# Kernel tuning notes

Measured on AMD Instinct MI355X. Metric: run time of the kernel, lower is better.

Reference implementation:

```python
import jax, jax.numpy as jnp
import numpy as np

N_STEPS = 25
H_DIM = 64


def _gru_cell(x_in, h, Wk, Uk, b):
    # Keras GRU v2 (reset_after=True):
    # x gates: x @ Wk + b[0]; h gates: h @ Uk + b[1]
    xg = x_in @ Wk + b[0]          # (B, 3H)
    hg = h @ Uk + b[1]             # (B, 3H)
    xz, xr, xh = jnp.split(xg, 3, axis=-1)
    hz, hr, hh = jnp.split(hg, 3, axis=-1)
    z = jax.nn.sigmoid(xz + hz)
    r = jax.nn.sigmoid(xr + hr)
    cand = jnp.tanh(xh + r * hh)
    return z * h + (1.0 - z) * cand


def setup_inputs() -> dict:
    key = jax.random.key(0)
    ks = jax.random.split(key, 6)
    B = 32768
    return {
        "x": jax.random.normal(ks[0], (B, 128), jnp.float32),
        "H": jax.random.normal(ks[1], (B, 64), jnp.float32),
        "Wk": jax.random.normal(ks[2], (128, 192), jnp.float32) * 0.05,
        "Uk": jax.random.normal(ks[3], (64, 192), jnp.float32) * 0.05,
        "b": jnp.zeros((2, 192), jnp.float32),
        "Wd": jax.random.normal(ks[4], (64, 78), jnp.float32) * 0.05,
        "bd": jnp.zeros((78,), jnp.float32),
    }


def reference(x, H, Wk, Uk, b, Wd, bd):
    # Step 0: 128-dim decoder input from x[1][:,0,0,:128].
    h1 = _gru_cell(x, H, Wk, Uk, b)
    # Steps 1..24: the 64-dim GRU output is fed back as the input; this is
    # equivalent to zero-padding it to 128 dims, i.e. using Wk[:64].
    Wk64 = Wk[:H_DIM]

    def body(h, _):
        hn = _gru_cell(h, h, Wk64, Uk, b)
        return hn, hn

    _, hs = jax.lax.scan(body, h1, None, length=N_STEPS - 1)  # (24, B, 64)
    outs = jnp.concatenate([h1[None], hs], axis=0)            # (25, B, 64)
    outs = jnp.transpose(outs, (1, 0, 2))                     # (B, 25, 64)
    logits = outs @ Wd + bd                                   # (B, 25, 78)
    return jax.nn.softmax(logits, axis=-1)
```

## Files before the change

### kernel.cpp

```cpp
#include <hip/hip_runtime.h>


typedef _Float16 f16x8 __attribute__((ext_vector_type(8)));
typedef float f32x4 __attribute__((ext_vector_type(4)));

#define TPB 512
#define LOG2E 1.44269504088896f
#define S2E   2.88539008177793f

template <int CTRL>
__device__ __forceinline__ float dppror(float x) {
  return __int_as_float(
      __builtin_amdgcn_update_dpp(0, __float_as_int(x), CTRL, 0xf, 0xf, true));
}
__device__ __forceinline__ void split8h(const float f[8], f16x8& hi, f16x8& lo) {
  #pragma unroll
  for (int j = 0; j < 8; ++j) {
    _Float16 h = (_Float16)f[j];
    hi[j] = h;
    lo[j] = (_Float16)(f[j] - (float)h);
  }
}

#define MFMA __builtin_amdgcn_mfma_f32_16x16x32_f16
#define EXP2 __builtin_amdgcn_exp2f
#define RCP  __builtin_amdgcn_rcpf

__global__ __launch_bounds__(TPB, 2) void vgru_all(
    const float* __restrict__ x, const float* __restrict__ Hin,
    const float* __restrict__ Wk, const float* __restrict__ Uk,
    const float* __restrict__ bias, const float* __restrict__ Wd,
    const float* __restrict__ bd, float* __restrict__ out)
{
  extern __shared__ float smem[];
  float* chkAll = smem;
  unsigned short* hs = (unsigned short*)(smem + 24576);

  const int tid  = threadIdx.x;
  const int lane = tid & 63, w = tid >> 6;
  const int g = lane >> 4, n = lane & 15;
  const int blockbase = blockIdx.x * 128;
  const int myrow0 = blockbase + w * 16;
  const float* b0 = bias;
  const float* b1 = bias + 192;

  float bb[16];
  #pragma unroll
  for (int jt = 0; jt < 4; ++jt) {
    int c = jt * 16 + n;
    bb[0 * 4 + jt] = (b0[c] + b1[c]) * LOG2E;
    bb[1 * 4 + jt] = (b0[64 + c] + b1[64 + c]) * LOG2E;
    bb[2 * 4 + jt] = b0[128 + c] * S2E;
    bb[3 * 4 + jt] = b1[128 + c] * S2E;
  }
  float bdv[5];
  #pragma unroll
  for (int nt = 0; nt < 5; ++nt) {
    int c = nt * 16 + n;
    bdv[nt] = (c < 78) ? bd[c] * LOG2E : 0.0f;
  }

  for (int idx = tid; idx < 96 * 64; idx += TPB) {
    int fi = idx >> 6, ln = idx & 63;
    int t = fi >> 4, ntb = fi & 15;
    int lg = ln >> 4, lnn = ln & 15;
    int c = ntb * 16 + lnn;
    float scale = (c < 128) ? LOG2E : S2E;
    f16x8 wf;
    #pragma unroll
    for (int j = 0; j < 8; ++j) {
      int k = t * 32 + lg * 8 + j;
      float v;
      if (k < 128) v = (c < 192) ? Wk[k * 192 + c] : 0.0f;
      else {
        int ku = k - 128;
        v = (c < 128) ? Uk[ku * 192 + c]
                      : ((c < 192) ? 0.0f : Uk[ku * 192 + 128 + (c - 192)]);
      }
      wf[j] = (_Float16)(v * scale);
    }
    ((f16x8*)chkAll)[fi * 64 + ln] = wf;
  }
  __syncthreads();

  f32x4 G0[16];
  #pragma unroll
  for (int ntb = 0; ntb < 16; ++ntb) {
    float bv = bb[ntb];
    G0[ntb] = (f32x4){bv, bv, bv, bv};
  }
  #pragma unroll 1
  for (int t = 0; t < 6; ++t) {
    f16x8 Ah, Al;
    {
      int row = myrow0 + n;
      const float* src = (t < 4)
          ? x + (size_t)row * 128 + t * 32 + g * 8
          : Hin + (size_t)row * 64 + (t - 4) * 32 + g * 8;
      float4 v0 = *(const float4*)src;
      float4 v1 = *(const float4*)(src + 4);
      float f[8] = {v0.x, v0.y, v0.z, v0.w, v1.x, v1.y, v1.z, v1.w};
      split8h(f, Ah, Al);
    }
    __builtin_amdgcn_s_setprio(1);
    #pragma unroll
    for (int ntb = 0; ntb < 16; ++ntb) {
      f16x8 wf = ((const f16x8*)chkAll)[(t * 16 + ntb) * 64 + lane];
      G0[ntb] = MFMA(Ah, wf, G0[ntb], 0, 0, 0);
      G0[ntb] = MFMA(Al, wf, G0[ntb], 0, 0, 0);
    }
    __builtin_amdgcn_s_setprio(0);
  }

  float hold[16];
  {
    unsigned short* h0 = hs + w * 2048;
    #pragma unroll
    for (int jt = 0; jt < 4; ++jt) {
      const int ksw = jt >> 1;
      const int gkw = (jt & 1) * 2 + (n >> 3);
      const int jw  = n & 7;
      #pragma unroll
      for (int rr = 0; rr < 4; ++rr) {
        int lrow = g * 4 + rr;
        float h0v = Hin[(size_t)(myrow0 + lrow) * 64 + jt * 16 + n];
        float z  = RCP(1.0f + EXP2(-G0[0 * 4 + jt][rr]));
        float rg = RCP(1.0f + EXP2(-G0[1 * 4 + jt][rr]));
        float y  = G0[2 * 4 + jt][rr] + rg * G0[3 * 4 + jt][rr];
        float cand = 1.0f - 2.0f * RCP(EXP2(y) + 1.0f);
        float hv = cand + z * (h0v - cand);
        hold[jt * 4 + rr] = hv;
        int off = ((ksw * 4 + gkw) * 16 + lrow) * 8 + jw;
        h0[off] = __builtin_bit_cast(unsigned short, (_Float16)hv);
      }
    }
  }
  __syncthreads();

  for (int idx = tid; idx < 2048; idx += TPB) {
    int fi = idx >> 6, ln = idx & 63;
    int ntb = fi >> 1, ks = fi & 1;
    int lg = ln >> 4, lnn = ln & 15;
    int c = ntb * 16 + lnn;
    float scale = (c < 128) ? LOG2E : S2E;
    f16x8 wf;
    #pragma unroll
    for (int j = 0; j < 8; ++j) {
      int k = ks * 32 + lg * 8 + j;
      float v;
      if      (c < 128) v = Wk[k * 192 + c] + Uk[k * 192 + c];
      else if (c < 192) v = Wk[k * 192 + c];
      else              v = Uk[k * 192 + 128 + (c - 192)];
      wf[j] = (_Float16)(v * scale);
    }
    ((f16x8*)smem)[fi * 64 + ln] = wf;
  }
  for (int idx = tid; idx < 640; idx += TPB) {
    int fi = idx >> 6, ln = idx & 63;
    int nt = fi >> 1, ks = fi & 1;
    int lg = ln >> 4, lnn = ln & 15;
    int c = nt * 16 + lnn;
    f16x8 wf;
    #pragma unroll
    for (int j = 0; j < 8; ++j) {
      int k = ks * 32 + lg * 8 + j;
      wf[j] = (_Float16)((c < 78) ? Wd[k * 78 + c] * LOG2E : 0.0f);
    }
    ((f16x8*)(smem + 8192))[fi * 64 + ln] = wf;
  }
  __syncthreads();

  const f16x8* GW = (const f16x8*)smem;
  f16x8 wdr[5][2];
  #pragma unroll
  for (int nt = 0; nt < 5; ++nt)
    #pragma unroll
    for (int ks = 0; ks < 2; ++ks)
      wdr[nt][ks] = ((const f16x8*)(smem + 8192))[(nt * 2 + ks) * 64 + lane];

  float* op0 = out + ((size_t)(myrow0 + g * 4 + 0) * 25) * 78 + n;
  float* op1 = out + ((size_t)(myrow0 + g * 4 + 1) * 25) * 78 + n;
  float* op2 = out + ((size_t)(myrow0 + g * 4 + 2) * 25) * 78 + n;
  float* op3 = out + ((size_t)(myrow0 + g * 4 + 3) * 25) * 78 + n;

  f16x8 Ah[2];
  {
    const unsigned short* c0 = hs + w * 2048;
    #pragma unroll
    for (int ks = 0; ks < 2; ++ks) {
      int off = ((ks * 4 + g) * 16 + n) * 8;
      Ah[ks] = *(const f16x8*)(c0 + off);
    }
  }

  #pragma unroll 1
  for (int s = 0; s < 25; ++s) {
    unsigned short* nxt = hs + w * 2048 + ((s + 1) & 1) * 1024;
    const bool last = (s == 24);

    f32x4 C[4][4];
    #pragma unroll
    for (int jt = 0; jt < 4; ++jt)
      #pragma unroll
      for (int gg = 0; gg < 4; ++gg) {
        float bv = bb[gg * 4 + jt];
        C[jt][gg] = (f32x4){bv, bv, bv, bv};
      }
    f32x4 L[5];
    #pragma unroll
    for (int nt = 0; nt < 5; ++nt)
      L[nt] = (f32x4){bdv[nt], bdv[nt], bdv[nt], bdv[nt]};

    __builtin_amdgcn_s_setprio(1);
    if (!last) {
      #pragma unroll
      for (int jt = 0; jt < 4; ++jt)
        #pragma unroll
        for (int ks = 0; ks < 2; ++ks) {
          f16x8 w0 = GW[((0 * 4 + jt) * 2 + ks) * 64 + lane];
          f16x8 w1 = GW[((1 * 4 + jt) * 2 + ks) * 64 + lane];
          f16x8 w2 = GW[((2 * 4 + jt) * 2 + ks) * 64 + lane];
          f16x8 w3 = GW[((3 * 4 + jt) * 2 + ks) * 64 + lane];
          C[jt][0] = MFMA(Ah[ks], w0, C[jt][0], 0, 0, 0);
          C[jt][1] = MFMA(Ah[ks], w1, C[jt][1], 0, 0, 0);
          C[jt][2] = MFMA(Ah[ks], w2, C[jt][2], 0, 0, 0);
          C[jt][3] = MFMA(Ah[ks], w3, C[jt][3], 0, 0, 0);
        }
    }
    #pragma unroll
    for (int nt = 0; nt < 5; ++nt)
      #pragma unroll
      for (int ks = 0; ks < 2; ++ks)
        L[nt] = MFMA(Ah[ks], wdr[nt][ks], L[nt], 0, 0, 0);
    __builtin_amdgcn_s_setprio(0);

    if (!last) {
      #pragma unroll
      for (int jt = 0; jt < 4; ++jt) {
        const int ksw = jt >> 1;
        const int gkw = (jt & 1) * 2 + (n >> 3);
        const int jw  = n & 7;
        #pragma unroll
        for (int rr = 0; rr < 4; ++rr) {
          float z  = RCP(1.0f + EXP2(-C[jt][0][rr]));
          float rg = RCP(1.0f + EXP2(-C[jt][1][rr]));
          float y  = C[jt][2][rr] + rg * C[jt][3][rr];
          float cand = 1.0f - 2.0f * RCP(EXP2(y) + 1.0f);
          float hv = cand + z * (hold[jt * 4 + rr] - cand);
          hold[jt * 4 + rr] = hv;
          int off = ((ksw * 4 + gkw) * 16 + (g * 4 + rr)) * 8 + jw;
          nxt[off] = __builtin_bit_cast(unsigned short, (_Float16)hv);
        }
      }
      #pragma unroll
      for (int ks = 0; ks < 2; ++ks) {
        int off = ((ks * 4 + g) * 16 + n) * 8;
        Ah[ks] = *(const f16x8*)(nxt + off);
      }
    }

    #pragma unroll
    for (int rr = 0; rr < 4; ++rr) {
      float e0 = EXP2(L[0][rr]);
      float e1 = EXP2(L[1][rr]);
      float e2 = EXP2(L[2][rr]);
      float e3 = EXP2(L[3][rr]);
      float e4 = (n < 14) ? EXP2(L[4][rr]) : 0.0f;
      float sm = e0 + e1 + e2 + e3 + e4;
      sm += dppror<0x128>(sm);
      sm += dppror<0x124>(sm);
      sm += dppror<0x122>(sm);
      sm += dppror<0x121>(sm);
      float inv = RCP(sm);
      float* orow = (rr == 0) ? op0 : (rr == 1) ? op1 : (rr == 2) ? op2 : op3;
      orow[0]  = e0 * inv;
      orow[16] = e1 * inv;
      orow[32] = e2 * inv;
      orow[48] = e3 * inv;
      if (n < 14) orow[64] = e4 * inv;
    }
    op0 += 78; op1 += 78; op2 += 78; op3 += 78;
  }
}

extern "C" void kernel_launch(void* const* d_in, const int* in_sizes, int n_in,
                              void* d_out, int out_size, void* d_ws, size_t ws_size,
                              hipStream_t stream) {
  const float* x   = (const float*)d_in[0];
  const float* H   = (const float*)d_in[1];
  const float* Wk  = (const float*)d_in[2];
  const float* Uk  = (const float*)d_in[3];
  const float* b   = (const float*)d_in[4];
  const float* Wd  = (const float*)d_in[5];
  const float* bd  = (const float*)d_in[6];
  float* out = (float*)d_out;
  (void)d_ws; (void)ws_size; (void)in_sizes; (void)n_in; (void)out_size;

  const int lds = 32768 * 4;
  hipFuncSetAttribute((const void*)vgru_all,
                      hipFuncAttributeMaxDynamicSharedMemorySize, lds);
  vgru_all<<<dim3(256), dim3(TPB), lds, stream>>>(x, H, Wk, Uk, b, Wd, bd, out);
}
```

Before: 112.5 us.

## Keep GRU recurrent weights in registers and split gate MFMAs into two halves

The 32 recurrent-gate weight fragments are loaded from shared memory into registers once, before the 25-step loop, instead of being re-read from LDS every step. The dense-layer weights, previously held in registers, are now read from LDS each step. Within a step, the gate MFMAs and activations are processed in two halves, so each half's transcendental math can overlap the other half's MFMAs and fewer accumulators are live at once. The cost is much higher VGPR use from 32 f16x8 weight registers, which may lower occupancy or cause spills.

```diff
diff --git a/kernel.cpp b/kernel.cpp
--- a/kernel.cpp
+++ b/kernel.cpp
@@ -91,7 +91,7 @@
   }
   #pragma unroll 1
   for (int t = 0; t < 6; ++t) {
-    f16x8 Ah, Al;
+    f16x8 Ah0, Al0;
     {
       int row = myrow0 + n;
       const float* src = (t < 4)
@@ -100,14 +100,14 @@
       float4 v0 = *(const float4*)src;
       float4 v1 = *(const float4*)(src + 4);
       float f[8] = {v0.x, v0.y, v0.z, v0.w, v1.x, v1.y, v1.z, v1.w};
-      split8h(f, Ah, Al);
+      split8h(f, Ah0, Al0);
     }
     __builtin_amdgcn_s_setprio(1);
     #pragma unroll
     for (int ntb = 0; ntb < 16; ++ntb) {
       f16x8 wf = ((const f16x8*)chkAll)[(t * 16 + ntb) * 64 + lane];
-      G0[ntb] = MFMA(Ah, wf, G0[ntb], 0, 0, 0);
-      G0[ntb] = MFMA(Al, wf, G0[ntb], 0, 0, 0);
+      G0[ntb] = MFMA(Ah0, wf, G0[ntb], 0, 0, 0);
+      G0[ntb] = MFMA(Al0, wf, G0[ntb], 0, 0, 0);
     }
     __builtin_amdgcn_s_setprio(0);
   }
@@ -170,13 +170,16 @@
   }
   __syncthreads();
 
-  const f16x8* GW = (const f16x8*)smem;
-  f16x8 wdr[5][2];
-  #pragma unroll
-  for (int nt = 0; nt < 5; ++nt)
-    #pragma unroll
-    for (int ks = 0; ks < 2; ++ks)
-      wdr[nt][ks] = ((const f16x8*)(smem + 8192))[(nt * 2 + ks) * 64 + lane];
+  f16x8 Wg[4][4][2];
+  #pragma unroll
+  for (int gg = 0; gg < 4; ++gg)
+    #pragma unroll
+    for (int jt = 0; jt < 4; ++jt)
+      #pragma unroll
+      for (int ks = 0; ks < 2; ++ks)
+        Wg[gg][jt][ks] = ((const f16x8*)smem)[((gg * 4 + jt) * 2 + ks) * 64 + lane];
+
+  const f16x8* WD = (const f16x8*)(smem + 8192);
 
   float* op0 = out + ((size_t)(myrow0 + g * 4 + 0) * 25) * 78 + n;
   float* op1 = out + ((size_t)(myrow0 + g * 4 + 1) * 25) * 78 + n;
@@ -198,58 +201,59 @@
     unsigned short* nxt = hs + w * 2048 + ((s + 1) & 1) * 1024;
     const bool last = (s == 24);
 
-    f32x4 C[4][4];
-    #pragma unroll
-    for (int jt = 0; jt < 4; ++jt)
-      #pragma unroll
-      for (int gg = 0; gg < 4; ++gg) {
-        float bv = bb[gg * 4 + jt];
-        C[jt][gg] = (f32x4){bv, bv, bv, bv};
-      }
     f32x4 L[5];
     #pragma unroll
     for (int nt = 0; nt < 5; ++nt)
       L[nt] = (f32x4){bdv[nt], bdv[nt], bdv[nt], bdv[nt]};
-
     __builtin_amdgcn_s_setprio(1);
+    #pragma unroll
+    for (int nt = 0; nt < 5; ++nt)
+      #pragma unroll
+      for (int ks = 0; ks < 2; ++ks)
+        L[nt] = MFMA(Ah[ks], WD[(nt * 2 + ks) * 64 + lane], L[nt], 0, 0, 0);
+    __builtin_amdgcn_s_setprio(0);
+
     if (!last) {
       #pragma unroll
-      for (int jt = 0; jt < 4; ++jt)
+      for (int jp = 0; jp < 2; ++jp) {
+        f32x4 C[2][4];
         #pragma unroll
-        for (int ks = 0; ks < 2; ++ks) {
-          f16x8 w0 = GW[((0 * 4 + jt) * 2 + ks) * 64 + lane];
-          f16x8 w1 = GW[((1 * 4 + jt) * 2 + ks) * 64 + lane];
-          f16x8 w2 = GW[((2 * 4 + jt) * 2 + ks) * 64 + lane];
-          f16x8 w3 = GW[((3 * 4 + jt) * 2 + ks) * 64 + lane];
-          C[jt][0] = MFMA(Ah[ks], w0, C[jt][0], 0, 0, 0);
-          C[jt][1] = MFMA(Ah[ks], w1, C[jt][1], 0, 0, 0);
-          C[jt][2] = MFMA(Ah[ks], w2, C[jt][2], 0, 0, 0);
-          C[jt][3] = MFMA(Ah[ks], w3, C[jt][3], 0, 0, 0);
+        for (int jl = 0; jl < 2; ++jl)
+          #pragma unroll
+          for (int gg = 0; gg < 4; ++gg) {
+            float bv = bb[gg * 4 + (jp * 2 + jl)];
+            C[jl][gg] = (f32x4){bv, bv, bv, bv};
+          }
+        __builtin_amdgcn_s_setprio(1);
+        #pragma unroll
+        for (int jl = 0; jl < 2; ++jl) {
+          const int jt = jp * 2 + jl;
+          #pragma unroll
+          for (int ks = 0; ks < 2; ++ks) {
+            C[jl][0] = MFMA(Ah[ks], Wg[0][jt][ks], C[jl][0], 0, 0, 0);
+            C[jl][1] = MFMA(Ah[ks], Wg[1][jt][ks], C[jl][1], 0, 0, 0);
+            C[jl][2] = MFMA(Ah[ks], Wg[2][jt][ks], C[jl][2], 0, 0, 0);
+            C[jl][3] = MFMA(Ah[ks], Wg[3][jt][ks], C[jl][3], 0, 0, 0);
+          }
         }
-    }
-    #pragma unroll
-    for (int nt = 0; nt < 5; ++nt)
-      #pragma unroll
-      for (int ks = 0; ks < 2; ++ks)
-        L[nt] = MFMA(Ah[ks], wdr[nt][ks], L[nt], 0, 0, 0);
-    __builtin_amdgcn_s_setprio(0);
-
-    if (!last) {
-      #pragma unroll
-      for (int jt = 0; jt < 4; ++jt) {
-        const int ksw = jt >> 1;
-        const int gkw = (jt & 1) * 2 + (n >> 3);
-        const int jw  = n & 7;
+        __builtin_amdgcn_s_setprio(0);
         #pragma unroll
-        for (int rr = 0; rr < 4; ++rr) {
-          float z  = RCP(1.0f + EXP2(-C[jt][0][rr]));
-          float rg = RCP(1.0f + EXP2(-C[jt][1][rr]));
-          float y  = C[jt][2][rr] + rg * C[jt][3][rr];
-          float cand = 1.0f - 2.0f * RCP(EXP2(y) + 1.0f);
-          float hv = cand + z * (hold[jt * 4 + rr] - cand);
-          hold[jt * 4 + rr] = hv;
-          int off = ((ksw * 4 + gkw) * 16 + (g * 4 + rr)) * 8 + jw;
-          nxt[off] = __builtin_bit_cast(unsigned short, (_Float16)hv);
+        for (int jl = 0; jl < 2; ++jl) {
+          const int jt = jp * 2 + jl;
+          const int ksw = jt >> 1;
+          const int gkw = (jt & 1) * 2 + (n >> 3);
+          const int jw  = n & 7;
+          #pragma unroll
+          for (int rr = 0; rr < 4; ++rr) {
+            float z  = RCP(1.0f + EXP2(-C[jl][0][rr]));
+            float rg = RCP(1.0f + EXP2(-C[jl][1][rr]));
+            float y  = C[jl][2][rr] + rg * C[jl][3][rr];
+            float cand = 1.0f - 2.0f * RCP(EXP2(y) + 1.0f);
+            float hv = cand + z * (hold[jt * 4 + rr] - cand);
+            hold[jt * 4 + rr] = hv;
+            int off = ((ksw * 4 + gkw) * 16 + (g * 4 + rr)) * 8 + jw;
+            nxt[off] = __builtin_bit_cast(unsigned short, (_Float16)hv);
+          }
         }
       }
       #pragma unroll
```

Result: slower. 221.2 us (+96.5%).
